# Optimization experiments

Measured on AMD Instinct MI355X. Metric: run time of the kernel, lower is better.

Reference implementation:

```python
import jax, jax.numpy as jnp
import numpy as np

N, E, F, H, G, C = 50000, 600000, 128, 128, 500, 10
BN_EPS = 1e-5

def setup_inputs() -> dict:
    key = jax.random.key(0)
    ks = jax.random.split(key, 20)
    def lin(k, fan_in, shape):
        b = 1.0 / np.sqrt(fan_in)
        return jax.random.uniform(k, shape, jnp.float32, -b, b)
    inp = {
        'x': jax.random.normal(ks[0], (N, F), jnp.float32),
        'edge_index': jax.random.randint(ks[1], (2, E), 0, N, jnp.int64),
        'batch': jnp.sort(jax.random.randint(ks[2], (N,), 0, G, jnp.int64)),
        # conv1 MLP: Linear(F,H) -> BN(H) -> ReLU -> Dropout -> Linear(H,H) -> ReLU
        'W1a': lin(ks[3], F, (F, H)), 'b1a': lin(ks[4], F, (H,)),
        'g1': jnp.ones((H,), jnp.float32), 'be1': jnp.zeros((H,), jnp.float32),
        'm1': jnp.zeros((H,), jnp.float32), 'v1': jnp.ones((H,), jnp.float32),
        'W1b': lin(ks[5], H, (H, H)), 'b1b': lin(ks[6], H, (H,)),
        # conv2 MLP: Linear(H,H) -> ReLU -> BN(H) -> Dropout -> Linear(H,H) -> ReLU
        'W2a': lin(ks[7], H, (H, H)), 'b2a': lin(ks[8], H, (H,)),
        'g2': jnp.ones((H,), jnp.float32), 'be2': jnp.zeros((H,), jnp.float32),
        'm2': jnp.zeros((H,), jnp.float32), 'v2': jnp.ones((H,), jnp.float32),
        'W2b': lin(ks[9], H, (H, H)), 'b2b': lin(ks[10], H, (H,)),
        # heads
        'Wl1': lin(ks[11], 2 * H, (2 * H, H // 2)), 'bl1': lin(ks[12], 2 * H, (H // 2,)),
        'Wl2': lin(ks[13], H // 2, (H // 2, C)), 'bl2': lin(ks[14], H // 2, (C,)),
    }
    return inp

def _bn(h, g, b, m, v):
    return (h - m) * (g / jnp.sqrt(v + BN_EPS)) + b

def _gin_aggregate(x, src, dst):
    # out[i] = x[i] + sum_{j->i} x[j]  (GINConv with eps=0)
    return x + jax.ops.segment_sum(x[src], dst, num_segments=N)

def reference(x, edge_index, batch,
              W1a, b1a, g1, be1, m1, v1, W1b, b1b,
              W2a, b2a, g2, be2, m2, v2, W2b, b2b,
              Wl1, bl1, Wl2, bl2):
    src, dst = edge_index[0], edge_index[1]
    # conv1
    a1 = _gin_aggregate(x, src, dst)                       # [N, F]
    h1 = _bn(a1 @ W1a + b1a, g1, be1, m1, v1)
    h1 = jax.nn.relu(h1)                                   # dropout = identity (eval)
    h1 = jax.nn.relu(h1 @ W1b + b1b)                       # [N, H]
    # conv2
    a2 = _gin_aggregate(h1, src, dst)                      # [N, H]
    h2 = jax.nn.relu(a2 @ W2a + b2a)
    h2 = _bn(h2, g2, be2, m2, v2)
    h2 = jax.nn.relu(h2 @ W2b + b2b)                       # [N, H]
    # global add pool per graph
    p1 = jax.ops.segment_sum(h1, batch, num_segments=G)    # [G, H]
    p2 = jax.ops.segment_sum(h2, batch, num_segments=G)    # [G, H]
    z = jnp.concatenate((p1, p2), axis=1)                  # [G, 2H]
    z = jax.nn.relu(z @ Wl1 + bl1)
    return z @ Wl2 + bl2                                   # [G, C]
```

## Files before the change

### kernel.cpp

```cpp
#include <hip/hip_runtime.h>

#define N_NODES 50000
#define N_EDGES 600000
#define HDIM 128
#define NGRAPH 500
#define NCLASS 10
#define BN_EPS 1e-5f
#define KSLOT 64
#define KSTRIDE 72

typedef short short8 __attribute__((ext_vector_type(8)));
typedef unsigned short ushort8v __attribute__((ext_vector_type(8)));
typedef float floatx4 __attribute__((ext_vector_type(4)));

__device__ __forceinline__ float bf2f(unsigned short u) {
    unsigned int v = ((unsigned int)u) << 16;
    return __uint_as_float(v);
}
__device__ __forceinline__ unsigned short f2bf(float f) {
    unsigned int u = __float_as_uint(f);
    unsigned int r = (u + 0x7fffu + ((u >> 16) & 1u)) >> 16;
    return (unsigned short)r;
}

__global__ void k_zero(int* __restrict__ cnt) {
    int i = blockIdx.x * blockDim.x + threadIdx.x;
    if (i < N_NODES) cnt[i] = 0;
}

#define ILV 13
#define NB_SCAT 586
#define NB_CAST 6250
#define NB_PREPW 256
#define NB_POOLZ 500
#define NB_SETUP (NB_SCAT * ILV)

__global__ void k_setup(const float* __restrict__ x, unsigned short* __restrict__ xb,
                        const int* __restrict__ src, const int* __restrict__ dst,
                        int* __restrict__ cnt, unsigned short* __restrict__ adj,
                        float* __restrict__ pool,
                        const float* __restrict__ W1a, const float* __restrict__ W1b,
                        const float* __restrict__ W2a, const float* __restrict__ W2b,
                        unsigned short* __restrict__ wpack,
                        const float* __restrict__ b1a, const float* __restrict__ g1,
                        const float* __restrict__ be1, const float* __restrict__ m1,
                        const float* __restrict__ v1, const float* __restrict__ b1b,
                        const float* __restrict__ b2a, const float* __restrict__ g2,
                        const float* __restrict__ be2, const float* __restrict__ m2,
                        const float* __restrict__ v2, const float* __restrict__ b2b,
                        float* __restrict__ ep) {
    int b = blockIdx.x;
    int t = threadIdx.x;
    if (b % ILV == 0) {
        int i4 = (b / ILV) * 256 + t;
        if (i4 < N_EDGES / 4) {
            int4 s4 = ((const int4*)src)[i4];
            int4 d4 = ((const int4*)dst)[i4];
            int p;
            p = atomicAdd(&cnt[d4.x], 1); if (p < KSLOT) adj[d4.x * KSTRIDE + p] = (unsigned short)s4.x;
            p = atomicAdd(&cnt[d4.y], 1); if (p < KSLOT) adj[d4.y * KSTRIDE + p] = (unsigned short)s4.y;
            p = atomicAdd(&cnt[d4.z], 1); if (p < KSLOT) adj[d4.z * KSTRIDE + p] = (unsigned short)s4.z;
            p = atomicAdd(&cnt[d4.w], 1); if (p < KSLOT) adj[d4.w * KSTRIDE + p] = (unsigned short)s4.w;
        }
        return;
    }
    b = b - b / ILV - 1;
    if (b < NB_CAST) {
        int i = b * 256 + t;
        float4 v = ((const float4*)x)[i];
        ushort4 o;
        o.x = f2bf(v.x); o.y = f2bf(v.y); o.z = f2bf(v.z); o.w = f2bf(v.w);
        ((ushort4*)xb)[i] = o;
        return;
    }
    b -= NB_CAST;
    if (b < NB_PREPW) {
        int e = b * 256 + t;
        int w = e >> 14;
        int s_ = e & 16383;
        int j = s_ & 7;
        int m = (s_ >> 3) & 15;
        int q = (s_ >> 7) & 3;
        int ks = (s_ >> 9) & 3;
        int ct = (s_ >> 11) & 7;
        int n = ct * 16 + m;
        int k;
        float scale = 1.f;
        if (w == 0 || w == 2) {
            k = ks * 32 + q * 8 + j;
        } else {
            k = (ks * 2 + (j >> 2)) * 16 + q * 4 + (j & 3);
            if (w == 3) scale = g2[k] * rsqrtf(v2[k] + BN_EPS);
        }
        const float* W = (w == 0) ? W1a : (w == 1) ? W1b : (w == 2) ? W2a : W2b;
        wpack[e] = f2bf(W[k * 128 + n] * scale);
        return;
    }
    b -= NB_PREPW;
    if (b < NB_POOLZ) {
        int i = b * 256 + t;
        pool[i] = 0.f;
        return;
    }
    b -= NB_POOLZ;
    if (b != 0) return;
    if (t < 128) {
        int j = t;
        float s1 = g1[j] * rsqrtf(v1[j] + BN_EPS);
        ep[0 * 256 + 0 + j]   = s1;
        ep[0 * 256 + 128 + j] = (b1a[j] - m1[j]) * s1 + be1[j];
        ep[1 * 256 + 0 + j]   = 1.f;
        ep[1 * 256 + 128 + j] = b2a[j];
        ep[512 + j] = b1b[j];
        float acc = b2b[j];
        for (int k = 0; k < 128; k++) {
            float s2k = g2[k] * rsqrtf(v2[k] + BN_EPS);
            acc += (be2[k] - m2[k] * s2k) * W2b[k * 128 + j];
        }
        ep[512 + 128 + j] = acc;
    }
}

__global__ __launch_bounds__(256) void k_agg(const unsigned short* __restrict__ x,
                                             const int* __restrict__ cnt,
                                             const unsigned short* __restrict__ adj,
                                             unsigned short* __restrict__ out) {
    int g = blockIdx.x * 256 + threadIdx.x;
    int node = g >> 4;
    int m = g & 15;
    if (node >= N_NODES) return;

    int len = cnt[node];
    if (len > KSLOT) len = KSLOT;
    const unsigned short* ad = adj + node * KSTRIDE;

    ushort8v ra = *(const ushort8v*)(ad);

    float self[8];
    {
        short8 sv = *(const short8*)(x + (size_t)node * 128 + m * 8);
        #pragma unroll
        for (int j = 0; j < 8; j++) self[j] = bf2f((unsigned short)sv[j]);
    }
    float acc[8];
    #pragma unroll
    for (int j = 0; j < 8; j++) acc[j] = self[j];

    int nb = (len + 7) >> 3;
    for (int b = 0; b < nb; b++) {
        int i = b * 8;
        ushort8v na = *(const ushort8v*)(ad + i + 8);
        int u0 = (i + 0 < len) ? (int)ra[0] : node;
        int u1 = (i + 1 < len) ? (int)ra[1] : node;
        int u2 = (i + 2 < len) ? (int)ra[2] : node;
        int u3 = (i + 3 < len) ? (int)ra[3] : node;
        int u4 = (i + 4 < len) ? (int)ra[4] : node;
        int u5 = (i + 5 < len) ? (int)ra[5] : node;
        int u6 = (i + 6 < len) ? (int)ra[6] : node;
        int u7 = (i + 7 < len) ? (int)ra[7] : node;
        short8 f0 = *(const short8*)(x + (size_t)u0 * 128 + m * 8);
        short8 f1 = *(const short8*)(x + (size_t)u1 * 128 + m * 8);
        short8 f2 = *(const short8*)(x + (size_t)u2 * 128 + m * 8);
        short8 f3 = *(const short8*)(x + (size_t)u3 * 128 + m * 8);
        short8 f4 = *(const short8*)(x + (size_t)u4 * 128 + m * 8);
        short8 f5 = *(const short8*)(x + (size_t)u5 * 128 + m * 8);
        short8 f6 = *(const short8*)(x + (size_t)u6 * 128 + m * 8);
        short8 f7 = *(const short8*)(x + (size_t)u7 * 128 + m * 8);
        #pragma unroll
        for (int j = 0; j < 8; j++) {
            float a = bf2f((unsigned short)f0[j]) + bf2f((unsigned short)f1[j]) +
                      bf2f((unsigned short)f2[j]) + bf2f((unsigned short)f3[j]);
            float c = bf2f((unsigned short)f4[j]) + bf2f((unsigned short)f5[j]) +
                      bf2f((unsigned short)f6[j]) + bf2f((unsigned short)f7[j]);
            acc[j] += a + c;
        }
        ra = na;
    }
    float extra = (float)(nb * 8 - len);
    #pragma unroll
    for (int j = 0; j < 8; j++) acc[j] -= extra * self[j];

    short8 r;
    #pragma unroll
    for (int j = 0; j < 8; j++) r[j] = (short)f2bf(acc[j]);
    *(short8*)(out + (size_t)node * 128 + m * 8) = r;
}

__global__ __launch_bounds__(256, 2) void k_mlp(const unsigned short* __restrict__ A,
                                                const unsigned short* __restrict__ WaP,
                                                const unsigned short* __restrict__ WbP,
                                                const float* __restrict__ epi,
                                                const float* __restrict__ epf,
                                                const int* __restrict__ batch,
                                                float* __restrict__ poolc,
                                                unsigned short* __restrict__ Out, int n) {
    __shared__ unsigned short Wl[2][16384];
    __shared__ float ps[16][132];
    int t = threadIdx.x;
    int lane = t & 63;
    int w = t >> 6;
    int q = lane >> 4;
    int m = lane & 15;

    int rowbase0 = blockIdx.x * 64;
    int base = rowbase0 + w * 16;
    int node = base + m;
    if (node >= n) node = n - 1;

    short8 a1[4];
    #pragma unroll
    for (int s = 0; s < 4; s++)
        a1[s] = *(const short8*)(A + (size_t)node * 128 + s * 32 + q * 8);

    #pragma unroll
    for (int i = 0; i < 8; i++) {
        int c = t + 256 * i;
        *(short8*)(&Wl[0][c * 8]) = *(const short8*)(WaP + c * 8);
        *(short8*)(&Wl[1][c * 8]) = *(const short8*)(WbP + c * 8);
    }
    __syncthreads();

    int lbase = lane * 8;

    floatx4 acc1[8];
    #pragma unroll
    for (int c = 0; c < 8; c++) acc1[c] = (floatx4)0.f;
    #pragma unroll
    for (int s = 0; s < 4; s++) {
        #pragma unroll
        for (int ct = 0; ct < 8; ct++) {
            short8 wf = *(const short8*)(&Wl[0][(ct * 4 + s) * 512 + lbase]);
            acc1[ct] = __builtin_amdgcn_mfma_f32_16x16x32_bf16(wf, a1[s], acc1[ct], 0, 0, 0);
        }
    }

    short8 a2[4];
    #pragma unroll
    for (int s = 0; s < 4; s++) {
        #pragma unroll
        for (int j = 0; j < 8; j++) {
            int ct = s * 2 + (j >> 2);
            int r = j & 3;
            int col = ct * 16 + q * 4 + r;
            float P = epi[col], Q = epi[128 + col];
            float v = fmaxf(fmaf(acc1[ct][r], P, Q), 0.f);
            a2[s][j] = (short)f2bf(v);
        }
    }

    floatx4 acc2[8];
    #pragma unroll
    for (int c = 0; c < 8; c++) acc2[c] = (floatx4)0.f;
    #pragma unroll
    for (int s = 0; s < 4; s++) {
        #pragma unroll
        for (int ct = 0; ct < 8; ct++) {
            short8 wf = *(const short8*)(&Wl[1][(ct * 4 + s) * 512 + lbase]);
            acc2[ct] = __builtin_amdgcn_mfma_f32_16x16x32_bf16(a2[s], wf, acc2[ct], 0, 0, 0);
        }
    }

    #pragma unroll
    for (int ct = 0; ct < 8; ct++) {
        float Qf = epf[ct * 16 + m];
        #pragma unroll
        for (int r = 0; r < 4; r++) acc2[ct][r] = fmaxf(acc2[ct][r] + Qf, 0.f);
    }

    if (Out) {
        #pragma unroll
        for (int ct = 0; ct < 8; ct++) {
            int col = ct * 16 + m;
            #pragma unroll
            for (int r = 0; r < 4; r++) {
                int gr = base + q * 4 + r;
                if (gr < n)
                    Out[(size_t)gr * 128 + col] = f2bf(acc2[ct][r]);
            }
        }
    }

    int mygid[4];
    #pragma unroll
    for (int r = 0; r < 4; r++) {
        int gr = base + q * 4 + r;
        mygid[r] = (gr < n) ? batch[gr] : -1;
    }
    int lastrow = rowbase0 + 63;
    if (lastrow > n - 1) lastrow = n - 1;
    int g0 = batch[rowbase0];
    int g1 = batch[lastrow];
    for (int g = g0; g <= g1; g++) {
        float pv[8];
        #pragma unroll
        for (int ct = 0; ct < 8; ct++) pv[ct] = 0.f;
        #pragma unroll
        for (int r = 0; r < 4; r++) {
            if (mygid[r] == g) {
                #pragma unroll
                for (int ct = 0; ct < 8; ct++) pv[ct] += acc2[ct][r];
            }
        }
        #pragma unroll
        for (int ct = 0; ct < 8; ct++) ps[w * 4 + q][ct * 16 + m] = pv[ct];
        __syncthreads();
        if (t < 128) {
            float s = 0.f;
            #pragma unroll
            for (int k = 0; k < 16; k++) s += ps[k][t];
            atomicAdd(&poolc[g * 256 + t], s);
        }
        __syncthreads();
    }
}

__global__ void k_head(const float* __restrict__ pool, const float* __restrict__ Wl1,
                       const float* __restrict__ bl1, const float* __restrict__ Wl2,
                       const float* __restrict__ bl2, float* __restrict__ out) {
    int g = blockIdx.x;
    int t = threadIdx.x;
    __shared__ float zmid[64];
    const float* z = pool + g * 256;
    float acc = bl1[t];
    #pragma unroll 8
    for (int k = 0; k < 256; k++) acc = fmaf(z[k], Wl1[k * 64 + t], acc);
    zmid[t] = fmaxf(acc, 0.f);
    __syncthreads();
    if (t < NCLASS) {
        float a = bl2[t];
        #pragma unroll
        for (int j = 0; j < 64; j++) a = fmaf(zmid[j], Wl2[j * 10 + t], a);
        out[g * NCLASS + t] = a;
    }
}


extern "C" void kernel_launch(void* const* d_in, const int* in_sizes, int n_in,
                              void* d_out, int out_size, void* d_ws, size_t ws_size,
                              hipStream_t stream) {
    const float* x   = (const float*)d_in[0];
    const int* eidx  = (const int*)d_in[1];
    const int* batch = (const int*)d_in[2];
    const float* W1a = (const float*)d_in[3];
    const float* b1a = (const float*)d_in[4];
    const float* g1  = (const float*)d_in[5];
    const float* be1 = (const float*)d_in[6];
    const float* m1  = (const float*)d_in[7];
    const float* v1  = (const float*)d_in[8];
    const float* W1b = (const float*)d_in[9];
    const float* b1b = (const float*)d_in[10];
    const float* W2a = (const float*)d_in[11];
    const float* b2a = (const float*)d_in[12];
    const float* g2  = (const float*)d_in[13];
    const float* be2 = (const float*)d_in[14];
    const float* m2  = (const float*)d_in[15];
    const float* v2  = (const float*)d_in[16];
    const float* W2b = (const float*)d_in[17];
    const float* b2b = (const float*)d_in[18];
    const float* Wl1 = (const float*)d_in[19];
    const float* bl1 = (const float*)d_in[20];
    const float* Wl2 = (const float*)d_in[21];
    const float* bl2 = (const float*)d_in[22];
    const int* srcv = eidx;
    const int* dstv = eidx + N_EDGES;

    char* ws = (char*)d_ws;
    size_t off = 0;
    auto alloc = [&](size_t bytes) -> void* {
        void* p = ws + off;
        off = (off + bytes + 255) & ~(size_t)255;
        return p;
    };
    int* cnt      = (int*)alloc(sizeof(int) * N_NODES);
    unsigned short* adj = (unsigned short*)alloc(sizeof(unsigned short) * (size_t)N_NODES * KSTRIDE);
    float* ep     = (float*)alloc(sizeof(float) * 768);
    float* pool   = (float*)alloc(sizeof(float) * NGRAPH * 256);
    unsigned short* wpack = (unsigned short*)alloc(sizeof(unsigned short) * 4 * 16384);
    unsigned short* xb    = (unsigned short*)alloc(sizeof(unsigned short) * (size_t)N_NODES * HDIM);
    unsigned short* bufA  = (unsigned short*)alloc(sizeof(unsigned short) * (size_t)N_NODES * HDIM);
    unsigned short* bufC  = (unsigned short*)alloc(sizeof(unsigned short) * (size_t)N_NODES * HDIM);
    (void)ws_size; (void)in_sizes; (void)n_in; (void)out_size;

    float* outp = (float*)d_out;

    k_zero<<<dim3((N_NODES + 255) / 256), dim3(256), 0, stream>>>(cnt);
    k_setup<<<dim3(NB_SETUP), dim3(256), 0, stream>>>(
        x, xb, srcv, dstv, cnt, adj, pool, W1a, W1b, W2a, W2b, wpack,
        b1a, g1, be1, m1, v1, b1b, b2a, g2, be2, m2, v2, b2b, ep);

    dim3 agrid((N_NODES * 16 + 255) / 256), ablk(256);
    dim3 mgrid((N_NODES + 63) / 64), mblk(256);

    k_agg<<<agrid, ablk, 0, stream>>>(xb, cnt, adj, bufA);
    k_mlp<<<mgrid, mblk, 0, stream>>>(bufA, wpack + 0 * 16384, wpack + 1 * 16384,
                                      ep + 0, ep + 512, batch, pool + 0, bufC, N_NODES);
    k_agg<<<agrid, ablk, 0, stream>>>(bufC, cnt, adj, bufA);
    k_mlp<<<mgrid, mblk, 0, stream>>>(bufA, wpack + 2 * 16384, wpack + 3 * 16384,
                                      ep + 256, ep + 640, batch, pool + 128, nullptr, N_NODES);
    k_head<<<dim3(NGRAPH), dim3(64), 0, stream>>>(pool, Wl1, bl1, Wl2, bl2, outp);
}
```

Measured before the change: 227.8 us.

## Replace zero kernel with memset and spread edge scatter across more blocks

Moves cnt and pool next to each other in the workspace and zeroes both with one hipMemsetAsync, replacing the separate k_zero kernel and the pool-zeroing blocks inside k_setup. The edge scatter now handles one edge per thread instead of four and is interleaved every 4th block rather than every 13th, spreading atomics over more blocks. The aim is to cut a launch and increase scatter parallelism; in exchange the scatter does narrower, non-vectorised loads, and the memset may itself be dispatched as a kernel.

```diff
diff --git a/kernel.cpp b/kernel.cpp
--- a/kernel.cpp
+++ b/kernel.cpp
@@ -23,22 +23,15 @@
     return (unsigned short)r;
 }
 
-__global__ void k_zero(int* __restrict__ cnt) {
-    int i = blockIdx.x * blockDim.x + threadIdx.x;
-    if (i < N_NODES) cnt[i] = 0;
-}
-
-#define ILV 13
-#define NB_SCAT 586
+#define ILV 4
+#define NB_SCAT 2344
 #define NB_CAST 6250
 #define NB_PREPW 256
-#define NB_POOLZ 500
 #define NB_SETUP (NB_SCAT * ILV)
 
 __global__ void k_setup(const float* __restrict__ x, unsigned short* __restrict__ xb,
                         const int* __restrict__ src, const int* __restrict__ dst,
                         int* __restrict__ cnt, unsigned short* __restrict__ adj,
-                        float* __restrict__ pool,
                         const float* __restrict__ W1a, const float* __restrict__ W1b,
                         const float* __restrict__ W2a, const float* __restrict__ W2b,
                         unsigned short* __restrict__ wpack,
@@ -51,16 +44,13 @@
                         float* __restrict__ ep) {
     int b = blockIdx.x;
     int t = threadIdx.x;
-    if (b % ILV == 0) {
-        int i4 = (b / ILV) * 256 + t;
-        if (i4 < N_EDGES / 4) {
-            int4 s4 = ((const int4*)src)[i4];
-            int4 d4 = ((const int4*)dst)[i4];
-            int p;
-            p = atomicAdd(&cnt[d4.x], 1); if (p < KSLOT) adj[d4.x * KSTRIDE + p] = (unsigned short)s4.x;
-            p = atomicAdd(&cnt[d4.y], 1); if (p < KSLOT) adj[d4.y * KSTRIDE + p] = (unsigned short)s4.y;
-            p = atomicAdd(&cnt[d4.z], 1); if (p < KSLOT) adj[d4.z * KSTRIDE + p] = (unsigned short)s4.z;
-            p = atomicAdd(&cnt[d4.w], 1); if (p < KSLOT) adj[d4.w * KSTRIDE + p] = (unsigned short)s4.w;
+    if ((b & (ILV - 1)) == 0) {
+        int i = (b >> 2) * 256 + t;
+        if (i < N_EDGES) {
+            int s = src[i];
+            int d = dst[i];
+            int p = atomicAdd(&cnt[d], 1);
+            if (p < KSLOT) adj[d * KSTRIDE + p] = (unsigned short)s;
         }
         return;
     }
@@ -97,12 +87,6 @@
         return;
     }
     b -= NB_PREPW;
-    if (b < NB_POOLZ) {
-        int i = b * 256 + t;
-        pool[i] = 0.f;
-        return;
-    }
-    b -= NB_POOLZ;
     if (b != 0) return;
     if (t < 128) {
         int j = t;
@@ -372,9 +356,10 @@
         return p;
     };
     int* cnt      = (int*)alloc(sizeof(int) * N_NODES);
+    float* pool   = (float*)alloc(sizeof(float) * NGRAPH * 256);
+    size_t zero_bytes = off;
     unsigned short* adj = (unsigned short*)alloc(sizeof(unsigned short) * (size_t)N_NODES * KSTRIDE);
     float* ep     = (float*)alloc(sizeof(float) * 768);
-    float* pool   = (float*)alloc(sizeof(float) * NGRAPH * 256);
     unsigned short* wpack = (unsigned short*)alloc(sizeof(unsigned short) * 4 * 16384);
     unsigned short* xb    = (unsigned short*)alloc(sizeof(unsigned short) * (size_t)N_NODES * HDIM);
     unsigned short* bufA  = (unsigned short*)alloc(sizeof(unsigned short) * (size_t)N_NODES * HDIM);
@@ -383,9 +368,9 @@
 
     float* outp = (float*)d_out;
 
-    k_zero<<<dim3((N_NODES + 255) / 256), dim3(256), 0, stream>>>(cnt);
+    hipMemsetAsync(ws, 0, zero_bytes, stream);
     k_setup<<<dim3(NB_SETUP), dim3(256), 0, stream>>>(
-        x, xb, srcv, dstv, cnt, adj, pool, W1a, W1b, W2a, W2b, wpack,
+        x, xb, srcv, dstv, cnt, adj, W1a, W1b, W2a, W2b, wpack,
         b1a, g1, be1, m1, v1, b1b, b2a, g2, be2, m2, v2, b2b, ep);
 
     dim3 agrid((N_NODES * 16 + 255) / 256), ablk(256);
```

New measurement: 231.4 us. About the same (+1.6%).
